# Performance work log

Measured on AMD Instinct MI355X. Metric: run time of the kernel, lower is better.

## Reference

```python
import jax, jax.numpy as jnp
import numpy as np

B, S, D, H = 4, 2048, 2048, 16
HD = D // H  # 128


def setup_inputs() -> dict:
    key = jax.random.key(0)
    k1, k2, k3 = jax.random.split(key, 3)
    sc = 1.0 / np.sqrt(D)
    return {
        "x": jax.random.normal(k1, (B, S, D), dtype=jnp.float32),
        "W_qkv": jax.random.normal(k2, (D, 3 * D), dtype=jnp.float32) * sc,
        "W_out": jax.random.normal(k3, (D, D), dtype=jnp.float32) * sc,
        "b_out": jnp.zeros((D,), dtype=jnp.float32),
    }


def _rotate_half(t):
    t1, t2 = jnp.split(t, 2, axis=-1)
    return jnp.concatenate([-t2, t1], axis=-1)


def reference(x, W_qkv, W_out, b_out):
    b, s, d = x.shape
    qkv = jnp.einsum('bsd,de->bse', x, W_qkv)  # fused QKV projection
    q, k, v = jnp.split(qkv, 3, axis=-1)
    # [b, h, s, hd]
    q = q.reshape(b, s, H, HD).transpose(0, 2, 1, 3)
    k = k.reshape(b, s, H, HD).transpose(0, 2, 1, 3)
    v = v.reshape(b, s, H, HD).transpose(0, 2, 1, 3)
    # RoPE (NeoX-style half-split), past_kv=None so positions = arange(s)
    pos = jnp.arange(s, dtype=jnp.float32)
    theta = 1.0 / (10000.0 ** (jnp.arange(0, HD, 2, dtype=jnp.float32) / HD))
    angles = pos[:, None] * theta[None, :]           # [s, hd/2]
    cos = jnp.concatenate([jnp.cos(angles)] * 2, -1)  # [s, hd] (repeat halves)
    sin = jnp.concatenate([jnp.sin(angles)] * 2, -1)
    cos = cos[None, None]  # [1,1,s,hd]
    sin = sin[None, None]
    q = q * cos + _rotate_half(q) * sin
    k = k * cos + _rotate_half(k) * sin
    # causal SDPA, scale = 1/sqrt(head_dim)
    scale = 1.0 / jnp.sqrt(jnp.asarray(HD, dtype=q.dtype))
    scores = jnp.einsum('bhqd,bhkd->bhqk', q, k) * scale
    causal = jnp.tril(jnp.ones((s, s), dtype=bool))
    scores = jnp.where(causal[None, None], scores, jnp.finfo(scores.dtype).min)
    attn = jax.nn.softmax(scores, axis=-1)
    out = jnp.einsum('bhqk,bhkd->bhqd', attn, v)
    out = out.transpose(0, 2, 1, 3).reshape(b, s, D)
    return jnp.einsum('bsd,de->bse', out, W_out) + b_out
```

## Files before the change

kernel.cpp:

```cpp
#include <hip/hip_runtime.h>

typedef unsigned short ushort_t;
typedef unsigned int u32;
typedef __attribute__((ext_vector_type(8))) short bf16x8;
typedef __attribute__((ext_vector_type(8))) unsigned short u16x8;
typedef __attribute__((ext_vector_type(4))) float f32x4;
typedef __attribute__((ext_vector_type(16))) float f32x16;

#define B_ 4
#define S_ 2048
#define D_ 2048
#define H_ 16
#define HD_ 128

__device__ __forceinline__ ushort_t f2bf(float f) {
  u32 x = __builtin_bit_cast(u32, f);
  x += 0x7fffu + ((x >> 16) & 1u);
  return (ushort_t)(x >> 16);
}
__device__ __forceinline__ float bf2f(ushort_t u) {
  u32 x = ((u32)u) << 16;
  return __builtin_bit_cast(float, x);
}

#define GLL16(srcp, ldsp)                                            \
  __builtin_amdgcn_global_load_lds(                                  \
      (const __attribute__((address_space(1))) u32*)(srcp),          \
      (__attribute__((address_space(3))) u32*)(ldsp), 16, 0, 0)

struct __align__(8) us4 { ushort_t x, y, z, w; };

__global__ void k_cvt_bf16(const float* __restrict__ in, ushort_t* __restrict__ out, int n) {
  int i = (blockIdx.x * 256 + threadIdx.x) * 4;
  if (i >= n) return;
  float4 v = *(const float4*)(in + i);
  us4 o;
  o.x = f2bf(v.x); o.y = f2bf(v.y); o.z = f2bf(v.z); o.w = f2bf(v.w);
  *(us4*)(out + i) = o;
}

__global__ void k_transpose_bf16(const float* __restrict__ in, ushort_t* __restrict__ out,
                                 int R, int C) {
  __shared__ float ld[32][33];
  int c0 = blockIdx.x * 32, r0 = blockIdx.y * 32;
  int tc = threadIdx.x & 31, tr = threadIdx.x >> 5;
#pragma unroll
  for (int i = 0; i < 4; ++i) {
    int r = tr + i * 8;
    ld[r][tc] = in[(size_t)(r0 + r) * C + c0 + tc];
  }
  __syncthreads();
#pragma unroll
  for (int i = 0; i < 4; ++i) {
    int r = tr + i * 8;
    out[(size_t)(c0 + r) * R + r0 + tc] = f2bf(ld[tc][r]);
  }
}

__global__ void k_rope_tables(float* __restrict__ cost, float* __restrict__ sint) {
  int i = blockIdx.x * 256 + threadIdx.x;
  int s = i >> 6, j = i & 63;
  double th = pow(10000.0, -(double)j / 64.0);
  double a = (double)s * th;
  cost[i] = (float)cos(a);
  sint[i] = (float)sin(a);
}

template <int MODE>
__global__ __launch_bounds__(512) void k_g8(const ushort_t* __restrict__ A,
                                            const ushort_t* __restrict__ Bt,
                                            void* __restrict__ Cout,
                                            const float* __restrict__ bias,
                                            int M, int N, int K) {
  __shared__ __attribute__((aligned(16))) ushort_t As[2][256 * 64];
  __shared__ __attribute__((aligned(16))) ushort_t Bs[2][256 * 64];
  const int tid = threadIdx.x;
  const int w = tid >> 6, l = tid & 63;
  const int l31 = l & 31, hl = l >> 5;
  const int wm = w >> 2, wn = w & 3;

  const int cpx = gridDim.x >> 3;
  const int bid = blockIdx.x;
  const int swzid = (bid & 7) * cpx + (bid >> 3);
  const int nbn = N >> 8;
  const size_t m0 = (size_t)(swzid / nbn) * 256;
  const size_t n0 = (size_t)(swzid % nbn) * 256;

  const size_t Kp = (size_t)K * 2;
  const char* Ab = (const char*)A + m0 * Kp;
  const char* Bb = (const char*)Bt + n0 * Kp;

  const int r0 = tid >> 3;
  const int ci16 = (tid & 7) * 16;
  const int sw0 = (((tid & 7) ^ (r0 & 7)) << 4);
  const int sw1 = (((tid & 7) ^ ((r0 + 64) & 7)) << 4);

#define STG_HALF(gbase, hrow, ldsbase, tcol)                                   \
  {                                                                            \
    GLL16((gbase) + (size_t)((hrow) + r0) * Kp + (tcol) + sw0,                 \
          (char*)(ldsbase) + ((hrow) + r0) * 128 + ci16);                      \
    GLL16((gbase) + (size_t)((hrow) + r0 + 64) * Kp + (tcol) + sw1,            \
          (char*)(ldsbase) + ((hrow) + r0 + 64) * 128 + ci16);                 \
  }

  f32x16 acc[4][2] = {};
  const int NI = K >> 7;

  const int arow = wm * 128 + l31;
  const int brow0 = wn * 64 + l31;

  STG_HALF(Ab, 0,   As[0], (size_t)0);
  STG_HALF(Ab, 128, As[0], (size_t)0);
  STG_HALF(Bb, 0,   Bs[0], (size_t)0);
  STG_HALF(Bb, 128, Bs[0], (size_t)0);
  STG_HALF(Bb, 0,   Bs[1], (size_t)128);
  STG_HALF(Bb, 128, Bs[1], (size_t)128);
  asm volatile("s_waitcnt vmcnt(4)");
  __builtin_amdgcn_sched_barrier(0);
  __builtin_amdgcn_s_barrier();

  for (int it = 0; it < NI; ++it) {
    const int t1 = 2 * it + 1;
    const bool more = (it + 1 < NI);
    const size_t cA1 = (size_t)t1 * 128;
    const size_t cT2 = (size_t)(t1 + 1) * 128;
    const size_t cT3 = (size_t)(t1 + 2) * 128;
    bf16x8 bq[2][4];
#pragma unroll
    for (int ph = 0; ph < 8; ++ph) {
      const int slot = ph >> 2;
      const int q = ph & 3;
      const char* Ac = (const char*)As[slot];
      const char* Bc = (const char*)Bs[slot];
      bf16x8 af[4];
      const int ar = arow + q * 32;
#pragma unroll
      for (int ks = 0; ks < 4; ++ks) {
        const int c = ks * 2 + hl;
        af[ks] = *(const bf16x8*)(Ac + ar * 128 + ((c ^ (ar & 7)) << 4));
      }
      if (q == 0) {
#pragma unroll
        for (int nt = 0; nt < 2; ++nt) {
          const int br = brow0 + nt * 32;
#pragma unroll
          for (int ks = 0; ks < 4; ++ks) {
            const int c = ks * 2 + hl;
            bq[nt][ks] = *(const bf16x8*)(Bc + br * 128 + ((c ^ (br & 7)) << 4));
          }
        }
      }
      if (ph == 0)      STG_HALF(Ab, 0,   As[1], cA1)
      else if (ph == 1) STG_HALF(Ab, 128, As[1], cA1)
      else if (ph == 2) { if (more) STG_HALF(Bb, 0,   Bs[0], cT2) }
      else if (ph == 3) { if (more) STG_HALF(Bb, 128, Bs[0], cT2) }
      else if (ph == 4) { if (more) STG_HALF(Ab, 0,   As[0], cT2) }
      else if (ph == 5) { if (more) STG_HALF(Ab, 128, As[0], cT2) }
      else if (ph == 6) { if (more) STG_HALF(Bb, 0,   Bs[1], cT3) }
      else              { if (more) STG_HALF(Bb, 128, Bs[1], cT3) }
      __builtin_amdgcn_s_barrier();
      asm volatile("s_waitcnt lgkmcnt(0)");
      __builtin_amdgcn_sched_barrier(0);
      __builtin_amdgcn_s_setprio(1);
#pragma unroll
      for (int ks = 0; ks < 4; ++ks) {
        acc[q][0] = __builtin_amdgcn_mfma_f32_32x32x16_bf16(af[ks], bq[0][ks], acc[q][0], 0, 0, 0);
        acc[q][1] = __builtin_amdgcn_mfma_f32_32x32x16_bf16(af[ks], bq[1][ks], acc[q][1], 0, 0, 0);
      }
      __builtin_amdgcn_s_setprio(0);
      if (ph == 3) {
        if (more) asm volatile("s_waitcnt vmcnt(4)");
        else      asm volatile("s_waitcnt vmcnt(0)");
        __builtin_amdgcn_sched_barrier(0);
      } else if (ph == 7 && more) {
        asm volatile("s_waitcnt vmcnt(4)");
        __builtin_amdgcn_sched_barrier(0);
      }
      __builtin_amdgcn_s_barrier();
    }
  }

  if (MODE == 2) {
#pragma unroll
    for (int nt = 0; nt < 2; ++nt) {
      const size_t col = n0 + wn * 64 + nt * 32 + l31;
      const float bia = bias[col];
#pragma unroll
      for (int mt = 0; mt < 4; ++mt)
#pragma unroll
        for (int r = 0; r < 16; ++r) {
          const size_t row = m0 + wm * 128 + mt * 32 + (r & 3) + 8 * (r >> 2) + 4 * hl;
          ((float*)Cout)[row * N + col] = acc[mt][nt][r] + bia;
        }
    }
  } else {
    ushort_t* Qbase = (ushort_t*)Cout;
#pragma unroll
    for (int nt = 0; nt < 2; ++nt) {
      const int col = (int)n0 + wn * 64 + nt * 32 + l31;
      const int p3 = col >> 11, rem = col & 2047;
      const int h = rem >> 7, d = rem & 127;
      ushort_t* base = Qbase + (size_t)p3 * 16777216ull + (size_t)h * (S_ * HD_) + d;
#pragma unroll
      for (int mt = 0; mt < 4; ++mt)
#pragma unroll
        for (int r = 0; r < 16; ++r) {
          const int row = (int)m0 + wm * 128 + mt * 32 + (r & 3) + 8 * (r >> 2) + 4 * hl;
          const int b2 = row >> 11, s = row & 2047;
          base[(size_t)b2 * (H_ * S_ * HD_) + (size_t)s * HD_] = f2bf(acc[mt][nt][r]);
        }
    }
  }
#undef STG_HALF
}

__global__ void k_rope2(ushort_t* __restrict__ t8, const float* __restrict__ cost,
                        const float* __restrict__ sint, float qscale) {
  int s0 = blockIdx.x * 32, h = blockIdx.y, b = blockIdx.z;
  int bh = b * H_ + h;
  const int t = threadIdx.x;
  const int sr = t >> 3, dj = (t & 7) * 8;
  const int s = s0 + sr;
  ushort_t* base = t8 + ((size_t)bh * S_ + s) * HD_;
  u16x8 lo = *(const u16x8*)(base + dj);
  u16x8 hi = *(const u16x8*)(base + 64 + dj);
  const float* cs = cost + s * 64 + dj;
  const float* sn = sint + s * 64 + dj;
  u16x8 olo, ohi;
#pragma unroll
  for (int j = 0; j < 8; ++j) {
    float fl = bf2f(lo[j]), fh = bf2f(hi[j]);
    float c = cs[j], sv = sn[j];
    olo[j] = f2bf((fl * c - fh * sv) * qscale);
    ohi[j] = f2bf((fh * c + fl * sv) * qscale);
  }
  *(u16x8*)(base + dj) = olo;
  *(u16x8*)(base + 64 + dj) = ohi;
}

__global__ void k_transT(const ushort_t* __restrict__ src, ushort_t* __restrict__ dst) {
  __shared__ ushort_t ld[32][33];
  int s0 = blockIdx.x * 32, d0 = blockIdx.y * 32, bh = blockIdx.z;
  const ushort_t* S = src + (size_t)bh * S_ * HD_;
  ushort_t* D = dst + (size_t)bh * HD_ * S_;
  const int tid = threadIdx.x;
#pragma unroll
  for (int i = 0; i < 4; ++i) {
    int e = i * 256 + tid;
    int sr = e >> 5, dc = e & 31;
    ld[sr][dc] = S[(size_t)(s0 + sr) * HD_ + d0 + dc];
  }
  __syncthreads();
#pragma unroll
  for (int i = 0; i < 4; ++i) {
    int e = i * 256 + tid;
    int dc = e >> 5, sr = e & 31;
    D[(size_t)(d0 + dc) * S_ + s0 + sr] = ld[sr][dc];
  }
}

__global__ __launch_bounds__(256, 2) void k_attn6(const ushort_t* __restrict__ Q,
                                                  const ushort_t* __restrict__ K,
                                                  const ushort_t* __restrict__ Vt,
                                                  ushort_t* __restrict__ O) {
  __shared__ __attribute__((aligned(16))) ushort_t Ks[2][64 * 128];
  __shared__ __attribute__((aligned(16))) ushort_t Vs[128 * 64];
  __shared__ __attribute__((aligned(16))) ushort_t Pl[8][16 * 72];

  const int id = blockIdx.x;
  const int work = (id & 7) * 128 + (id >> 3);
  const int bh = work >> 4;
  const int qt = 15 - (work & 15);
  const int b = bh >> 4, h = bh & 15;

  const int tid = threadIdx.x;
  const int w = tid >> 6, l = tid & 63;
  const int lr = l & 15, lg = l >> 4;
  const int qb = qt * 128 + w * 32;

  const ushort_t* Qp = Q + (size_t)bh * S_ * HD_;
  const char* Kpb = (const char*)(K + (size_t)bh * S_ * HD_);
  const char* Vpb = (const char*)(Vt + (size_t)bh * HD_ * S_);

  int kr[4], ksz[4], vr[4], vsz[4];
#pragma unroll
  for (int r = 0; r < 4; ++r) {
    int c = r * 256 + tid;
    kr[r] = c >> 4;
    ksz[r] = (((c & 15) ^ (kr[r] & 15)) << 4);
    vr[r] = c >> 3;
    vsz[r] = (((c & 7) ^ (vr[r] & 7)) << 4);
  }

#define STAGE_K(kb_, bufi)                                                       \
  {                                                                              \
    _Pragma("unroll") for (int r = 0; r < 4; ++r)                                \
        GLL16(Kpb + (size_t)((kb_) + kr[r]) * 256 + ksz[r],                      \
              (char*)Ks[bufi] + (size_t)(r * 256 + tid) * 16);                   \
  }
#define STAGE_V(kb_)                                                             \
  {                                                                              \
    _Pragma("unroll") for (int r = 0; r < 4; ++r)                                \
        GLL16(Vpb + (size_t)vr[r] * (S_ * 2) + (size_t)(kb_) * 2 + vsz[r],       \
              (char*)Vs + (size_t)(r * 256 + tid) * 16);                         \
  }

  bf16x8 qf[2][4];
#pragma unroll
  for (int f = 0; f < 2; ++f)
#pragma unroll
    for (int dw = 0; dw < 4; ++dw)
      qf[f][dw] = *(const bf16x8*)(Qp + (size_t)(qb + f * 16 + lr) * HD_ + dw * 32 + lg * 8);

  f32x4 oacc[2][8] = {};
  float lsum[2] = {0.f, 0.f};
  const int nkt = 2 * qt + 2;

  STAGE_K(0, 0);
  for (int kt = 0; kt < nkt; ++kt) {
    const int kb = kt * 64;
    const int cur = kt & 1;
    const bool morek = (kt + 1 < nkt);
    if (morek) STAGE_K(kb + 64, cur ^ 1);
    STAGE_V(kb);
    if (morek) asm volatile("s_waitcnt vmcnt(8)");
    else       asm volatile("s_waitcnt vmcnt(4)");
    __builtin_amdgcn_sched_barrier(0);
    __builtin_amdgcn_s_barrier();

    const bool live = (kb <= qb + 31);
    f32x4 st[2][4];
    if (live) {
      const char* Kc = (const char*)Ks[cur];
      __builtin_amdgcn_s_setprio(1);
#pragma unroll
      for (int t = 0; t < 4; ++t) {
        bf16x8 kf[4];
#pragma unroll
        for (int dw = 0; dw < 4; ++dw)
          kf[dw] = *(const bf16x8*)(Kc + (t * 16 + lr) * 256 + (((dw * 4 + lg) ^ lr) << 4));
        f32x4 a0 = {}, a1 = {};
#pragma unroll
        for (int dw = 0; dw < 4; ++dw) {
          a0 = __builtin_amdgcn_mfma_f32_16x16x32_bf16(kf[dw], qf[0][dw], a0, 0, 0, 0);
          a1 = __builtin_amdgcn_mfma_f32_16x16x32_bf16(kf[dw], qf[1][dw], a1, 0, 0, 0);
        }
        st[0][t] = a0;
        st[1][t] = a1;
      }
      __builtin_amdgcn_s_setprio(0);

#pragma unroll
      for (int f = 0; f < 2; ++f) {
        const int qg = qb + f * 16 + lr;
        const bool full = (kb + 63) <= (qb + f * 16);
        if (!full) {
#pragma unroll
          for (int t = 0; t < 4; ++t)
#pragma unroll
            for (int j = 0; j < 4; ++j) {
              int kg = kb + t * 16 + lg * 4 + j;
              st[f][t][j] = (kg > qg) ? -1e30f : st[f][t][j];
            }
        }
        float psum = 0.f;
        ushort_t* Pw = (ushort_t*)Pl[w * 2 + f];
#pragma unroll
        for (int t = 0; t < 4; ++t) {
          float p0 = exp2f(st[f][t][0]);
          float p1 = exp2f(st[f][t][1]);
          float p2 = exp2f(st[f][t][2]);
          float p3 = exp2f(st[f][t][3]);
          psum += (p0 + p1) + (p2 + p3);
          u32 pk0, pk1;
          asm("v_cvt_pk_bf16_f32 %0, %1, %2" : "=v"(pk0) : "v"(p0), "v"(p1));
          asm("v_cvt_pk_bf16_f32 %0, %1, %2" : "=v"(pk1) : "v"(p2), "v"(p3));
          *(u32*)&Pw[lr * 72 + t * 16 + lg * 4] = pk0;
          *(u32*)&Pw[lr * 72 + t * 16 + lg * 4 + 2] = pk1;
        }
        lsum[f] += psum;
      }
    }
    if (morek) asm volatile("s_waitcnt vmcnt(4)");
    else       asm volatile("s_waitcnt vmcnt(0)");
    __builtin_amdgcn_sched_barrier(0);
    __builtin_amdgcn_s_barrier();

    if (live) {
      __builtin_amdgcn_s_setprio(1);
#pragma unroll
      for (int kw = 0; kw < 2; ++kw) {
        bf16x8 pa0 = *(const bf16x8*)&Pl[w * 2 + 0][lr * 72 + kw * 32 + lg * 8];
        bf16x8 pa1 = *(const bf16x8*)&Pl[w * 2 + 1][lr * 72 + kw * 32 + lg * 8];
#pragma unroll
        for (int dt = 0; dt < 8; ++dt) {
          bf16x8 vf = *(const bf16x8*)((const char*)Vs + (dt * 16 + lr) * 128 +
                                       (((kw * 4 + lg) ^ (lr & 7)) << 4));
          oacc[0][dt] = __builtin_amdgcn_mfma_f32_16x16x32_bf16(pa0, vf, oacc[0][dt], 0, 0, 0);
          oacc[1][dt] = __builtin_amdgcn_mfma_f32_16x16x32_bf16(pa1, vf, oacc[1][dt], 0, 0, 0);
        }
      }
      __builtin_amdgcn_s_setprio(0);
    }
    __builtin_amdgcn_s_barrier();
  }

#pragma unroll
  for (int f = 0; f < 2; ++f) {
    lsum[f] += __shfl_xor(lsum[f], 16, 64);
    lsum[f] += __shfl_xor(lsum[f], 32, 64);
    float l0 = __shfl(lsum[f], lg * 4 + 0, 64);
    float l1 = __shfl(lsum[f], lg * 4 + 1, 64);
    float l2 = __shfl(lsum[f], lg * 4 + 2, 64);
    float l3 = __shfl(lsum[f], lg * 4 + 3, 64);
    float i0 = 1.f / l0, i1 = 1.f / l1, i2 = 1.f / l2, i3 = 1.f / l3;
    ushort_t* Op = O + (size_t)(b * S_ + qb + f * 16) * D_ + h * HD_;
#pragma unroll
    for (int dt = 0; dt < 8; ++dt) {
      Op[(size_t)(lg * 4 + 0) * D_ + dt * 16 + lr] = f2bf(oacc[f][dt][0] * i0);
      Op[(size_t)(lg * 4 + 1) * D_ + dt * 16 + lr] = f2bf(oacc[f][dt][1] * i1);
      Op[(size_t)(lg * 4 + 2) * D_ + dt * 16 + lr] = f2bf(oacc[f][dt][2] * i2);
      Op[(size_t)(lg * 4 + 3) * D_ + dt * 16 + lr] = f2bf(oacc[f][dt][3] * i3);
    }
  }
#undef STAGE_K
#undef STAGE_V
}

extern "C" void kernel_launch(void* const* d_in, const int* in_sizes, int n_in,
                              void* d_out, int out_size, void* d_ws, size_t ws_size,
                              hipStream_t stream) {
  const float* x = (const float*)d_in[0];
  const float* Wqkv = (const float*)d_in[1];
  const float* Wout = (const float*)d_in[2];
  const float* bout = (const float*)d_in[3];
  char* ws = (char*)d_ws;

  ushort_t* xb  = (ushort_t*)(ws + 0);
  ushort_t* Wqt = (ushort_t*)(ws + 33554432ull);
  ushort_t* Qr  = (ushort_t*)(ws + 58720256ull);
  ushort_t* Kr  = (ushort_t*)(ws + 92274688ull);
  ushort_t* Vr  = (ushort_t*)(ws + 125829120ull);
  ushort_t* Vt  = (ushort_t*)(ws + 159383552ull);
  float* cost   = (float*)(ws + 192937984ull);
  float* sint   = (float*)(ws + 193462272ull);

  const int M = B_ * S_;
  const float kSc = 0.08838834764831845f * 1.4426950408889634f;

  k_cvt_bf16<<<dim3((M * D_) / 4 / 256), 256, 0, stream>>>(x, xb, M * D_);
  k_transpose_bf16<<<dim3(3 * D_ / 32, D_ / 32), 256, 0, stream>>>(Wqkv, Wqt, D_, 3 * D_);
  k_rope_tables<<<dim3(S_ * 64 / 256), 256, 0, stream>>>(cost, sint);

  k_g8<1><<<dim3((M / 256) * (3 * D_ / 256)), 512, 0, stream>>>(
      xb, Wqt, Qr, nullptr, M, 3 * D_, D_);

  k_rope2<<<dim3(S_ / 32, H_, B_), 256, 0, stream>>>(Qr, cost, sint, kSc);
  k_rope2<<<dim3(S_ / 32, H_, B_), 256, 0, stream>>>(Kr, cost, sint, 1.0f);
  k_transT<<<dim3(S_ / 32, HD_ / 32, B_ * H_), 256, 0, stream>>>(Vr, Vt);

  k_transpose_bf16<<<dim3(D_ / 32, D_ / 32), 256, 0, stream>>>(Wout, Vr, D_, D_);

  k_attn6<<<dim3((S_ / 128) * B_ * H_), 256, 0, stream>>>(Qr, Kr, Vt, xb );

  k_g8<2><<<dim3((M / 256) * (D_ / 256)), 512, 0, stream>>>(
      xb, Vr, d_out, bout, M, D_, D_);
}
```

Measured before the change: 500.8 us.

## Load V fragments directly into registers and drop the LDS staging barrier

The attention kernel stops staging V tiles through shared memory. Each wave now reads its V fragments straight from global memory into registers: the first half before the QK^T step, the second half after it. This removes the V shared buffer and the second block barrier per key tile. The freed LDS lets launch bounds rise to three blocks per CU. The cost is that every wave fetches the same V data separately, so global/L2 traffic and register pressure go up, and the hand-written vmcnt waits must match the new load counts.

```diff
diff --git a/kernel.cpp b/kernel.cpp
--- a/kernel.cpp
+++ b/kernel.cpp
@@ -259,12 +259,11 @@
   }
 }
 
-__global__ __launch_bounds__(256, 2) void k_attn6(const ushort_t* __restrict__ Q,
+__global__ __launch_bounds__(256, 3) void k_attn7(const ushort_t* __restrict__ Q,
                                                   const ushort_t* __restrict__ K,
                                                   const ushort_t* __restrict__ Vt,
                                                   ushort_t* __restrict__ O) {
   __shared__ __attribute__((aligned(16))) ushort_t Ks[2][64 * 128];
-  __shared__ __attribute__((aligned(16))) ushort_t Vs[128 * 64];
   __shared__ __attribute__((aligned(16))) ushort_t Pl[8][16 * 72];
 
   const int id = blockIdx.x;
@@ -280,16 +279,14 @@
 
   const ushort_t* Qp = Q + (size_t)bh * S_ * HD_;
   const char* Kpb = (const char*)(K + (size_t)bh * S_ * HD_);
-  const char* Vpb = (const char*)(Vt + (size_t)bh * HD_ * S_);
-
-  int kr[4], ksz[4], vr[4], vsz[4];
+  const ushort_t* Vp = Vt + (size_t)bh * HD_ * S_;
+
+  int kr[4], ksz[4];
 #pragma unroll
   for (int r = 0; r < 4; ++r) {
     int c = r * 256 + tid;
     kr[r] = c >> 4;
     ksz[r] = (((c & 15) ^ (kr[r] & 15)) << 4);
-    vr[r] = c >> 3;
-    vsz[r] = (((c & 7) ^ (vr[r] & 7)) << 4);
   }
 
 #define STAGE_K(kb_, bufi)                                                       \
@@ -298,12 +295,6 @@
         GLL16(Kpb + (size_t)((kb_) + kr[r]) * 256 + ksz[r],                      \
               (char*)Ks[bufi] + (size_t)(r * 256 + tid) * 16);                   \
   }
-#define STAGE_V(kb_)                                                             \
-  {                                                                              \
-    _Pragma("unroll") for (int r = 0; r < 4; ++r)                                \
-        GLL16(Vpb + (size_t)vr[r] * (S_ * 2) + (size_t)(kb_) * 2 + vsz[r],       \
-              (char*)Vs + (size_t)(r * 256 + tid) * 16);                         \
-  }
 
   bf16x8 qf[2][4];
 #pragma unroll
@@ -321,17 +312,28 @@
     const int kb = kt * 64;
     const int cur = kt & 1;
     const bool morek = (kt + 1 < nkt);
+    const bool live = (kb <= qb + 31);
+
+    bf16x8 v0[8];
+    if (live) {
+#pragma unroll
+      for (int dt = 0; dt < 8; ++dt)
+        v0[dt] = *(const bf16x8*)(Vp + (size_t)(dt * 16 + lr) * S_ + kb + lg * 8);
+    }
     if (morek) STAGE_K(kb + 64, cur ^ 1);
-    STAGE_V(kb);
-    if (morek) asm volatile("s_waitcnt vmcnt(8)");
-    else       asm volatile("s_waitcnt vmcnt(4)");
+    if (live) {
+      if (morek) asm volatile("s_waitcnt vmcnt(16)");
+      else       asm volatile("s_waitcnt vmcnt(8)");
+    } else {
+      if (morek) asm volatile("s_waitcnt vmcnt(8)");
+      else       asm volatile("s_waitcnt vmcnt(0)");
+    }
     __builtin_amdgcn_sched_barrier(0);
     __builtin_amdgcn_s_barrier();
 
-    const bool live = (kb <= qb + 31);
-    f32x4 st[2][4];
     if (live) {
       const char* Kc = (const char*)Ks[cur];
+      f32x4 st[2][4];
       __builtin_amdgcn_s_setprio(1);
 #pragma unroll
       for (int t = 0; t < 4; ++t) {
@@ -349,6 +351,11 @@
         st[1][t] = a1;
       }
       __builtin_amdgcn_s_setprio(0);
+
+      bf16x8 v1[8];
+#pragma unroll
+      for (int dt = 0; dt < 8; ++dt)
+        v1[dt] = *(const bf16x8*)(Vp + (size_t)(dt * 16 + lr) * S_ + kb + 32 + lg * 8);
 
 #pragma unroll
       for (int f = 0; f < 2; ++f) {
@@ -380,24 +387,24 @@
         }
         lsum[f] += psum;
       }
-    }
-    if (morek) asm volatile("s_waitcnt vmcnt(4)");
-    else       asm volatile("s_waitcnt vmcnt(0)");
-    __builtin_amdgcn_sched_barrier(0);
-    __builtin_amdgcn_s_barrier();
-
-    if (live) {
+
       __builtin_amdgcn_s_setprio(1);
-#pragma unroll
-      for (int kw = 0; kw < 2; ++kw) {
-        bf16x8 pa0 = *(const bf16x8*)&Pl[w * 2 + 0][lr * 72 + kw * 32 + lg * 8];
-        bf16x8 pa1 = *(const bf16x8*)&Pl[w * 2 + 1][lr * 72 + kw * 32 + lg * 8];
+      {
+        bf16x8 pa0 = *(const bf16x8*)&Pl[w * 2 + 0][lr * 72 + lg * 8];
+        bf16x8 pa1 = *(const bf16x8*)&Pl[w * 2 + 1][lr * 72 + lg * 8];
 #pragma unroll
         for (int dt = 0; dt < 8; ++dt) {
-          bf16x8 vf = *(const bf16x8*)((const char*)Vs + (dt * 16 + lr) * 128 +
-                                       (((kw * 4 + lg) ^ (lr & 7)) << 4));
-          oacc[0][dt] = __builtin_amdgcn_mfma_f32_16x16x32_bf16(pa0, vf, oacc[0][dt], 0, 0, 0);
-          oacc[1][dt] = __builtin_amdgcn_mfma_f32_16x16x32_bf16(pa1, vf, oacc[1][dt], 0, 0, 0);
+          oacc[0][dt] = __builtin_amdgcn_mfma_f32_16x16x32_bf16(pa0, v0[dt], oacc[0][dt], 0, 0, 0);
+          oacc[1][dt] = __builtin_amdgcn_mfma_f32_16x16x32_bf16(pa1, v0[dt], oacc[1][dt], 0, 0, 0);
+        }
+      }
+      {
+        bf16x8 pa0 = *(const bf16x8*)&Pl[w * 2 + 0][lr * 72 + 32 + lg * 8];
+        bf16x8 pa1 = *(const bf16x8*)&Pl[w * 2 + 1][lr * 72 + 32 + lg * 8];
+#pragma unroll
+        for (int dt = 0; dt < 8; ++dt) {
+          oacc[0][dt] = __builtin_amdgcn_mfma_f32_16x16x32_bf16(pa0, v1[dt], oacc[0][dt], 0, 0, 0);
+          oacc[1][dt] = __builtin_amdgcn_mfma_f32_16x16x32_bf16(pa1, v1[dt], oacc[1][dt], 0, 0, 0);
         }
       }
       __builtin_amdgcn_s_setprio(0);
@@ -424,7 +431,6 @@
     }
   }
 #undef STAGE_K
-#undef STAGE_V
 }
 
 extern "C" void kernel_launch(void* const* d_in, const int* in_sizes, int n_in,
@@ -461,7 +467,7 @@
 
   k_transpose_bf16<<<dim3(D_ / 32, D_ / 32), 256, 0, stream>>>(Wout, Vr, D_, D_);
 
-  k_attn6<<<dim3((S_ / 128) * B_ * H_), 256, 0, stream>>>(Qr, Kr, Vt, xb );
+  k_attn7<<<dim3((S_ / 128) * B_ * H_), 256, 0, stream>>>(Qr, Kr, Vt, xb );
 
   k_g8<2><<<dim3((M / 256) * (D_ / 256)), 512, 0, stream>>>(
       xb, Vr, d_out, bout, M, D_, D_);
```

Result: slower. 954.0 us (+90.5%).
